# Kernel tuning notes

Measured on AMD Instinct MI355X. Metric: run time of the kernel, lower is better.

## Reference

```python
import jax, jax.numpy as jnp
import numpy as np

B, S, D, H = 2, 2048, 2048, 16
HD = D // H  # 128


def apply_rotary(xq, xk, cos, sin):
    # xq, xk: [B, S, H, HD]; cos, sin: [S, HD//2]
    def rot(x):
        xr = x.astype(jnp.float32).reshape(*x.shape[:-1], -1, 2)  # [B,S,H,HD/2,2]
        xe, xo = xr[..., 0], xr[..., 1]
        c = cos[None, :, None, :]
        s = sin[None, :, None, :]
        out_e = xe * c - xo * s
        out_o = xe * s + xo * c
        out = jnp.stack([out_e, out_o], axis=-1).reshape(x.shape)
        return out.astype(x.dtype)
    return rot(xq), rot(xk)


def setup_inputs() -> dict:
    key = jax.random.key(0)
    ks = jax.random.split(key, 8)
    x = jax.random.normal(ks[0], (B, S, D), dtype=jnp.float32)
    scale = 1.0 / np.sqrt(D)
    wq = jax.random.normal(ks[1], (D, D), dtype=jnp.float32) * scale
    wk = jax.random.normal(ks[2], (D, D), dtype=jnp.float32) * scale
    wv = jax.random.normal(ks[3], (D, D), dtype=jnp.float32) * scale
    wo = jax.random.normal(ks[4], (D, D), dtype=jnp.float32) * scale
    # RoPE frequencies (standard LLaMA): theta = 10000
    inv_freq = 1.0 / (10000.0 ** (np.arange(0, HD, 2, dtype=np.float32) / HD))
    t = np.arange(S, dtype=np.float32)
    ang = np.outer(t, inv_freq)  # [S, HD/2]
    freqs_cos = jnp.asarray(np.cos(ang))
    freqs_sin = jnp.asarray(np.sin(ang))
    # causal additive mask [1,1,S,S]
    neg = jnp.full((S, S), -1e9, dtype=jnp.float32)
    mask = jnp.triu(neg, k=1)[None, None, :, :]
    return {"x": x, "start_pos": 0, "freqs_cos": freqs_cos, "freqs_sin": freqs_sin,
            "mask": mask, "wq": wq, "wk": wk, "wv": wv, "wo": wo}


def reference(x, start_pos, freqs_cos, freqs_sin, mask, wq, wk, wv, wo):
    bsz, seqlen, dim = x.shape
    xq = (x @ wq.T).reshape(bsz, seqlen, H, HD)
    xk = (x @ wk.T).reshape(bsz, seqlen, H, HD)
    xv = (x @ wv.T).reshape(bsz, seqlen, H, HD)
    xq, xk = apply_rotary(xq, xk, freqs_cos, freqs_sin)
    # [B,H,S,HD]
    q = xq.transpose(0, 2, 1, 3)
    k = xk.transpose(0, 2, 1, 3)
    v = xv.transpose(0, 2, 1, 3)
    scores = jnp.einsum('bhqd,bhkd->bhqk', q, k) / jnp.sqrt(jnp.float32(HD))
    scores = scores + mask
    probs = jax.nn.softmax(scores.astype(jnp.float32), axis=-1).astype(q.dtype)
    out = jnp.einsum('bhqk,bhkd->bhqd', probs, v)
    out = out.transpose(0, 2, 1, 3).reshape(bsz, seqlen, dim)
    return out @ wo.T
```

## Files before the change

kernel.cpp:

```cpp
#include <hip/hip_runtime.h>
#include <cstdint>

typedef unsigned short u16;
typedef __attribute__((ext_vector_type(8))) short bf16x8;
typedef __attribute__((ext_vector_type(4))) float f32x4;

#define S_LEN 2048
#define DM    2048
#define NH    16
#define HDIM  128

__device__ __forceinline__ u16 f2bf(float f) {
  union { float f; unsigned u; } v; v.f = f;
  unsigned r = v.u + 0x7fffu + ((v.u >> 16) & 1u);
  return (u16)(r >> 16);
}
__device__ __forceinline__ float bf2f(u16 h) {
  union { unsigned u; float f; } v; v.u = ((unsigned)h) << 16;
  return v.f;
}

typedef __attribute__((address_space(3))) void lds_void_t;
typedef const __attribute__((address_space(1))) void gbl_void_t;
__device__ __forceinline__ void gload_lds16(const void* g, void* l) {
  __builtin_amdgcn_global_load_lds((gbl_void_t*)g, (lds_void_t*)l, 16, 0, 0);
}

#define VMCNTN(nn) asm volatile("s_waitcnt vmcnt(%0)" :: "n"(nn) : "memory")

__global__ void cvt5_k(const float* s0, u16* d0, int n0,
                       const float* s1, u16* d1, int n1,
                       const float* s2, u16* d2, int n2,
                       const float* s3, u16* d3, int n3,
                       const float* s4, u16* d4, int n4) {
  const int stride = gridDim.x * blockDim.x;
  const int tid = blockIdx.x * blockDim.x + threadIdx.x;
#define CVT(S, D, N)                                        \
  for (int i = tid; i < ((N) >> 2); i += stride) {          \
    float4 v = ((const float4*)(S))[i];                     \
    ushort4 o;                                              \
    o.x = f2bf(v.x); o.y = f2bf(v.y);                       \
    o.z = f2bf(v.z); o.w = f2bf(v.w);                       \
    ((ushort4*)(D))[i] = o;                                 \
  }
  CVT(s0, d0, n0) CVT(s1, d1, n1) CVT(s2, d2, n2)
  CVT(s3, d3, n3) CVT(s4, d4, n4)
#undef CVT
}

template <int BM, int BN, int M, int N, int K, typename CT, int MODE>
__global__ __launch_bounds__(512, 2) void gemm8(const u16* __restrict__ A,
                                                const u16* __restrict__ Bm,
                                                CT* __restrict__ C,
                                                const float* __restrict__ fc,
                                                const float* __restrict__ fs,
                                                u16* __restrict__ qtp,
                                                u16* __restrict__ ktp) {
  constexpr int PWM = BM / 2, PWN = BN / 4;
  constexpr int MR = PWM / 16, NR = PWN / 16, NB = NR / 2;
  constexpr int LA = BM / 128, LB = BN / 128;
  constexpr int VM = LA + LB;
  constexpr int nbn = N / BN, nbm = M / BM;
  constexpr int nwg = nbm * nbn;
  constexpr int GM = 8;
  __shared__ u16 sA[4 * BM * 32];
  __shared__ u16 sB[4 * BN * 32];

  const int t = threadIdx.x;
  const int lane = t & 63, wid = t >> 6;
  const int r0 = lane & 15, kq = lane >> 4;
  const int wr = wid >> 2, wc = wid & 3;

  const int bid = blockIdx.x;
  const int wgl = (bid & 7) * (nwg >> 3) + (bid >> 3);
  const int gid = wgl / (GM * nbn);
  const int rem = wgl % (GM * nbn);
  const long tile_m = (long)(gid * GM + (rem & (GM - 1))) * BM;
  const long tile_n = (long)(rem >> 3) * BN;

  constexpr int NT = K >> 6;
  constexpr int NITER = NT >> 1;

  const int swzcol = ((t & 3) ^ ((t >> 3) & 3)) * 8;
  const u16* gA = A + (tile_m + (t >> 2)) * (long)K + swzcol;
  const u16* gB = Bm + (tile_n + (t >> 2)) * (long)K + swzcol;

  auto stageA = [&](int kt, int kh) {
    u16* base = &sA[((kt & 1) * 2 + kh) * (BM * 32)] + wid * 512;
#pragma unroll
    for (int r = 0; r < LA; ++r)
      gload_lds16(gA + (long)(r * 128) * K + kt * 64 + kh * 32, base + r * 4096);
  };
  auto stageB = [&](int kt, int kh) {
    u16* base = &sB[((kt & 1) * 2 + kh) * (BN * 32)] + wid * 512;
#pragma unroll
    for (int r = 0; r < LB; ++r)
      gload_lds16(gB + (long)(r * 128) * K + kt * 64 + kh * 32, base + r * 4096);
  };

  const int rdslot = (kq ^ ((r0 >> 1) & 3)) * 8;
  const int aoff = (wr * PWM + r0) * 32 + rdslot;
  const int boff = (wc * PWN + r0) * 32 + rdslot;

  f32x4 acc[MR][NR];
#pragma unroll
  for (int m = 0; m < MR; ++m)
#pragma unroll
    for (int n = 0; n < NR; ++n) acc[m][n] = (f32x4){0.f, 0.f, 0.f, 0.f};

  stageA(0, 0); stageB(0, 0); stageA(0, 1); stageB(0, 1);
  stageA(1, 0); stageB(1, 0);
  VMCNTN(VM);
  __builtin_amdgcn_s_barrier();

#define PH(KT, KH, G, STAGE_STMT, VM_STMT)                                  \
  {                                                                         \
    const u16* ra = &sA[(((KT) & 1) * 2 + (KH)) * (BM * 32)] + aoff;        \
    const u16* rb = &sB[(((KT) & 1) * 2 + (KH)) * (BN * 32)] + boff;        \
    if ((G) == 0) {                                                         \
      _Pragma("unroll") for (int m = 0; m < MR; ++m)                        \
          a[m] = *(const bf16x8*)(ra + m * 512);                            \
    }                                                                       \
    _Pragma("unroll") for (int n = 0; n < NB; ++n)                          \
        b[n] = *(const bf16x8*)(rb + ((G) * NB + n) * 512);                 \
    STAGE_STMT;                                                             \
    VM_STMT;                                                                \
    __builtin_amdgcn_s_barrier();                                           \
    __builtin_amdgcn_s_setprio(1);                                          \
    _Pragma("unroll") for (int m = 0; m < MR; ++m)                          \
        _Pragma("unroll") for (int n = 0; n < NB; ++n)                      \
            acc[m][(G) * NB + n] = __builtin_amdgcn_mfma_f32_16x16x32_bf16( \
                a[m], b[n], acc[m][(G) * NB + n], 0, 0, 0);                 \
    __builtin_amdgcn_s_setprio(0);                                          \
    __builtin_amdgcn_s_barrier();                                           \
  }

  for (int it = 0; it < NITER; ++it) {
    const int kt0 = 2 * it, kt1 = 2 * it + 1;
    const bool last = (it == NITER - 1);
    bf16x8 a[MR], b[NB];
    PH(kt0, 0, 0, stageA(kt1, 1), ((void)0));
    PH(kt0, 0, 1, stageB(kt1, 1), ((void)0));
    PH(kt0, 1, 0, { if (kt0 + 2 < NT) stageA(kt0 + 2, 0); }, ((void)0));
    PH(kt0, 1, 1, { if (kt0 + 2 < NT) stageB(kt0 + 2, 0); },
       { if (last) { VMCNTN(0); } else { VMCNTN(VM); } });
    PH(kt1, 0, 0, { if (kt0 + 2 < NT) stageA(kt0 + 2, 1); }, ((void)0));
    PH(kt1, 0, 1, { if (kt0 + 2 < NT) stageB(kt0 + 2, 1); }, ((void)0));
    PH(kt1, 1, 0, { if (kt0 + 3 < NT) stageA(kt0 + 3, 0); }, ((void)0));
    PH(kt1, 1, 1, { if (kt0 + 3 < NT) stageB(kt0 + 3, 0); }, VMCNTN(VM));
  }
#undef PH

  if constexpr (MODE == 1) {
    const int z = (int)(tile_n >> 11);
    if (z == 2) {
#pragma unroll
      for (int m = 0; m < MR; ++m)
#pragma unroll
        for (int n = 0; n < NR; ++n)
#pragma unroll
          for (int r = 0; r < 4; ++r) {
            long grow = tile_m + wr * PWM + m * 16 + kq * 4 + r;
            long gcol = tile_n + wc * PWN + n * 16 + r0;
            C[grow * N + gcol] = (CT)f2bf(acc[m][n][r]);
          }
    } else {
      const float qsc = 0.12751743202f;
#pragma unroll
      for (int m = 0; m < MR; ++m)
#pragma unroll
        for (int n = 0; n < NR; ++n)
#pragma unroll
          for (int r = 0; r < 4; ++r) {
            long grow = tile_m + wr * PWM + m * 16 + kq * 4 + r;
            long gcol = tile_n + wc * PWN + n * 16 + r0;
            int srow = (int)(grow & 2047), bidx = (int)(grow >> 11);
            int h = ((int)gcol >> 7) & 15, hd = (int)gcol & 127;
            float v = acc[m][n][r];
            float partner = __shfl_xor(v, 1);
            int hd2 = hd >> 1;
            float c = fc[srow * 64 + hd2], sn = fs[srow * 64 + hd2];
            float res = (r0 & 1) ? (partner * sn + v * c)
                                 : (v * c - partner * sn);
            if (z == 0) res *= qsc;
            u16* dst = z ? ktp : qtp;
            dst[((long)(bidx * 16 + h) * S_LEN + srow) * HDIM + hd] = f2bf(res);
          }
    }
  } else {
#pragma unroll
    for (int m = 0; m < MR; ++m)
#pragma unroll
      for (int n = 0; n < NR; ++n)
#pragma unroll
        for (int r = 0; r < 4; ++r) {
          long grow = tile_m + wr * PWM + m * 16 + kq * 4 + r;
          long gcol = tile_n + wc * PWN + n * 16 + r0;
          float v = acc[m][n][r];
          if constexpr (sizeof(CT) == 2) C[grow * N + gcol] = (CT)f2bf(v);
          else                           C[grow * N + gcol] = v;
        }
  }
}

__global__ void vtrans_k(const u16* __restrict__ qkv, u16* __restrict__ vt) {
  __shared__ u16 tile[64][65];
  int bh = blockIdx.z;
  int b = bh >> 4, h = bh & 15;
  int s0 = blockIdx.x * 64, d0 = blockIdx.y * 64;
  int tx = threadIdx.x, ty = threadIdx.y;
#pragma unroll
  for (int i = 0; i < 64; i += 4) {
    int s = s0 + ty + i;
    tile[ty + i][tx] = qkv[((long)(b * S_LEN + s)) * 6144 + 4096 + h * HDIM + d0 + tx];
  }
  __syncthreads();
#pragma unroll
  for (int i = 0; i < 64; i += 4) {
    int d = d0 + ty + i;
    vt[((long)bh * HDIM + d) * S_LEN + s0 + tx] = tile[tx][ty + i];
  }
}

__global__ __launch_bounds__(128) void flash_k(const u16* __restrict__ qt,
                                               const u16* __restrict__ kt,
                                               const u16* __restrict__ vt,
                                               u16* __restrict__ attn) {
  constexpr int PS = 40;
  __shared__ u16 pbuf[2][2][32 * PS];
  const int t = threadIdx.x, lane = t & 63, wid = t >> 6;
  const int r0 = lane & 15, kq = lane >> 4;
  const int bh = blockIdx.x, b = bh >> 4, h = bh & 15;
  const int tile = (gridDim.y - 1) - blockIdx.y;
  const int q0w = tile * 64 + wid * 32;
  const int crow = kq * 4;

  const u16* qb = qt + ((long)bh * S_LEN + q0w) * HDIM;
  const u16* kb = kt + (long)bh * S_LEN * HDIM;
  const u16* vb = vt + (long)bh * HDIM * S_LEN;
  u16* pb0 = &pbuf[0][wid][0];
  u16* pb1 = &pbuf[1][wid][0];

  bf16x8 aq[2][4];
#pragma unroll
  for (int qc = 0; qc < 2; ++qc)
#pragma unroll
    for (int kk = 0; kk < 4; ++kk)
      aq[qc][kk] = *(const bf16x8*)(qb + (qc * 16 + r0) * HDIM + kk * 32 + kq * 8);

  f32x4 o[2][8];
  float mrow[2] = {-1e30f, -1e30f}, lrow[2] = {0.f, 0.f};
#pragma unroll
  for (int qc = 0; qc < 2; ++qc)
#pragma unroll
    for (int dt = 0; dt < 8; ++dt) o[qc][dt] = (f32x4){0.f, 0.f, 0.f, 0.f};

  bf16x8 bkA[2][4], bkB[2][4], bvA[8], bvB[8];
  f32x4 saccA[2][2], saccB[2][2];

  auto loadK = [&](bf16x8 (&dst)[2][4], int kv) {
#pragma unroll
    for (int kc = 0; kc < 2; ++kc)
#pragma unroll
      for (int kk = 0; kk < 4; ++kk)
        dst[kc][kk] = *(const bf16x8*)(kb + (long)(kv + kc * 16 + r0) * HDIM + kk * 32 + kq * 8);
  };
  auto loadV = [&](bf16x8 (&dst)[8], int kv) {
#pragma unroll
    for (int dt = 0; dt < 8; ++dt)
      dst[dt] = *(const bf16x8*)(vb + (long)(dt * 16 + r0) * S_LEN + kv + kq * 8);
  };
  auto qk = [&](bf16x8 (&kf)[2][4], f32x4 (&sacc)[2][2]) {
    __builtin_amdgcn_s_setprio(1);
#pragma unroll
    for (int kc = 0; kc < 2; ++kc) {
      f32x4 a0 = (f32x4){0.f, 0.f, 0.f, 0.f};
      f32x4 a1 = (f32x4){0.f, 0.f, 0.f, 0.f};
#pragma unroll
      for (int kk = 0; kk < 4; ++kk) {
        a0 = __builtin_amdgcn_mfma_f32_16x16x32_bf16(kf[kc][kk], aq[0][kk], a0, 0, 0, 0);
        a1 = __builtin_amdgcn_mfma_f32_16x16x32_bf16(kf[kc][kk], aq[1][kk], a1, 0, 0, 0);
      }
      sacc[kc][0] = a0; sacc[kc][1] = a1;
    }
    __builtin_amdgcn_s_setprio(0);
  };
  auto softmax_store = [&](f32x4 (&sacc)[2][2], int kv0, u16* pb) {
    const bool diag = (kv0 == q0w);
#pragma unroll
    for (int qc = 0; qc < 2; ++qc) {
      float s[2][4];
#pragma unroll
      for (int kc = 0; kc < 2; ++kc)
#pragma unroll
        for (int r = 0; r < 4; ++r) {
          float v = sacc[kc][qc][r];
          if (diag && (kc * 16 + crow + r > qc * 16 + r0)) v = -1e30f;
          s[kc][r] = v;
        }
      float pm = fmaxf(fmaxf(fmaxf(s[0][0], s[0][1]), fmaxf(s[0][2], s[0][3])),
                       fmaxf(fmaxf(s[1][0], s[1][1]), fmaxf(s[1][2], s[1][3])));
      pm = fmaxf(pm, __shfl_xor(pm, 16));
      pm = fmaxf(pm, __shfl_xor(pm, 32));
      if (!__all(pm - mrow[qc] <= 11.5416f)) {
        float mnew = fmaxf(mrow[qc], pm);
        float co = exp2f(mrow[qc] - mnew);
        mrow[qc] = mnew;
        lrow[qc] *= co;
        float cod[4];
#pragma unroll
        for (int r = 0; r < 4; ++r)
          cod[r] = __shfl(co, (lane & 48) | (crow + r));
#pragma unroll
        for (int dt = 0; dt < 8; ++dt)
#pragma unroll
          for (int r = 0; r < 4; ++r)
            o[qc][dt][r] *= cod[r];
      }
      float p[2][4];
      float rs = 0.f;
#pragma unroll
      for (int kc = 0; kc < 2; ++kc)
#pragma unroll
        for (int r = 0; r < 4; ++r) {
          p[kc][r] = exp2f(s[kc][r] - mrow[qc]);
          rs += p[kc][r];
        }
      rs += __shfl_xor(rs, 16);
      rs += __shfl_xor(rs, 32);
      lrow[qc] += rs;
#pragma unroll
      for (int kc = 0; kc < 2; ++kc) {
        unsigned w0, w1;
        asm("v_cvt_pk_bf16_f32 %0, %1, %2" : "=v"(w0) : "v"(p[kc][0]), "v"(p[kc][1]));
        asm("v_cvt_pk_bf16_f32 %0, %1, %2" : "=v"(w1) : "v"(p[kc][2]), "v"(p[kc][3]));
        uint2 w; w.x = w0; w.y = w1;
        *(uint2*)(pb + (qc * 16 + r0) * PS + kc * 16 + crow) = w;
      }
    }
  };
  auto pv = [&](const u16* pb, bf16x8 (&bv)[8]) {
    bf16x8 pa0 = *(const bf16x8*)(pb + r0 * PS + kq * 8);
    bf16x8 pa1 = *(const bf16x8*)(pb + (16 + r0) * PS + kq * 8);
    __builtin_amdgcn_s_setprio(1);
#pragma unroll
    for (int dt = 0; dt < 8; ++dt) {
      o[0][dt] = __builtin_amdgcn_mfma_f32_16x16x32_bf16(pa0, bv[dt], o[0][dt], 0, 0, 0);
      o[1][dt] = __builtin_amdgcn_mfma_f32_16x16x32_bf16(pa1, bv[dt], o[1][dt], 0, 0, 0);
    }
    __builtin_amdgcn_s_setprio(0);
  };

  loadK(bkA, 0);
  if (32 <= q0w) loadK(bkB, 32);
  qk(bkA, saccA);
  int kv0 = 0;
  for (;;) {
    {
      const bool more = (kv0 + 32 <= q0w);
      loadV(bvA, kv0);
      softmax_store(saccA, kv0, pb0);
      if (more) qk(bkB, saccB);
      if (kv0 + 64 <= q0w) loadK(bkA, kv0 + 64);
      pv(pb0, bvA);
      kv0 += 32;
      if (!more) break;
    }
    {
      const bool more = (kv0 + 32 <= q0w);
      loadV(bvB, kv0);
      softmax_store(saccB, kv0, pb1);
      if (more) qk(bkA, saccA);
      if (kv0 + 64 <= q0w) loadK(bkB, kv0 + 64);
      pv(pb1, bvB);
      kv0 += 32;
      if (!more) break;
    }
  }

#pragma unroll
  for (int qc = 0; qc < 2; ++qc) {
    float linv[4];
#pragma unroll
    for (int r = 0; r < 4; ++r)
      linv[r] = 1.0f / __shfl(lrow[qc], (lane & 48) | (crow + r));
#pragma unroll
    for (int dt = 0; dt < 8; ++dt)
#pragma unroll
      for (int r = 0; r < 4; ++r) {
        int srow = q0w + qc * 16 + crow + r;
        attn[((long)(b * S_LEN + srow)) * DM + h * HDIM + dt * 16 + r0] =
            f2bf(o[qc][dt][r] * linv[r]);
      }
  }
}

extern "C" void kernel_launch(void* const* d_in, const int* in_sizes, int n_in,
                              void* d_out, int out_size, void* d_ws, size_t ws_size,
                              hipStream_t stream) {
  (void)in_sizes; (void)n_in; (void)out_size; (void)ws_size;
  const float* x  = (const float*)d_in[0];
  const float* fc = (const float*)d_in[2];
  const float* fs = (const float*)d_in[3];
  const float* wq = (const float*)d_in[5];
  const float* wk = (const float*)d_in[6];
  const float* wv = (const float*)d_in[7];
  const float* wo = (const float*)d_in[8];
  float* out = (float*)d_out;

  u16* xb   = (u16*)d_ws;
  u16* wqkv = xb + 8388608;
  u16* wob  = wqkv + 12582912;
  u16* qkv  = wob + 4194304;
  u16* qt   = qkv + 25165824;
  u16* kt   = qt + 8388608;
  u16* vt   = kt + 8388608;
  u16* attn = qkv;

  cvt5_k<<<2048, 256, 0, stream>>>(x, xb, 8388608,
                                   wq, wqkv, 4194304,
                                   wk, wqkv + 4194304, 4194304,
                                   wv, wqkv + 8388608, 4194304,
                                   wo, wob, 4194304);

  gemm8<128, 256, 4096, 6144, 2048, u16, 1><<<768, 512, 0, stream>>>(
      xb, wqkv, qkv, fc, fs, qt, kt);

  vtrans_k<<<dim3(32, 2, 32), dim3(64, 4), 0, stream>>>(qkv, vt);

  flash_k<<<dim3(32, 32), 128, 0, stream>>>(qt, kt, vt, attn);

  gemm8<128, 256, 4096, 2048, 2048, float, 0><<<256, 512, 0, stream>>>(
      attn, wob, out, nullptr, nullptr, nullptr, nullptr);
}
```

Baseline: 316.9 us.

## Merge GEMM main-loop half-phases into four full-width phases with deeper prefetch

The GEMM main loop is restructured from eight half-width phases per iteration (each loading half the B fragments and staging one of A or B) into four full-width phases. Each phase now loads all A and B fragments, stages both A and B for a future k-slice, and waits with a larger outstanding-load count. This halves the number of barriers per iteration and keeps more global loads in flight. In exchange it doubles the live B fragment registers under a 512-thread, 2-block launch bound, which risks spills. It also drops the end-of-K bounds checks and the final full drain, so the last iterations issue prefetches past K.

```diff
diff --git a/kernel.cpp b/kernel.cpp
--- a/kernel.cpp
+++ b/kernel.cpp
@@ -57,9 +57,9 @@
                                                 u16* __restrict__ qtp,
                                                 u16* __restrict__ ktp) {
   constexpr int PWM = BM / 2, PWN = BN / 4;
-  constexpr int MR = PWM / 16, NR = PWN / 16, NB = NR / 2;
+  constexpr int MR = PWM / 16, NR = PWN / 16;
   constexpr int LA = BM / 128, LB = BN / 128;
-  constexpr int VM = LA + LB;
+  constexpr int VM6 = 2 * (LA + LB);
   constexpr int nbn = N / BN, nbm = M / BM;
   constexpr int nwg = nbm * nbn;
   constexpr int GM = 8;
@@ -110,46 +110,39 @@
 
   stageA(0, 0); stageB(0, 0); stageA(0, 1); stageB(0, 1);
   stageA(1, 0); stageB(1, 0);
-  VMCNTN(VM);
+  VMCNTN(VM6);
   __builtin_amdgcn_s_barrier();
 
-#define PH(KT, KH, G, STAGE_STMT, VM_STMT)                                  \
+#define PH4(KT, KH, SKT, SKH)                                               \
   {                                                                         \
     const u16* ra = &sA[(((KT) & 1) * 2 + (KH)) * (BM * 32)] + aoff;        \
     const u16* rb = &sB[(((KT) & 1) * 2 + (KH)) * (BN * 32)] + boff;        \
-    if ((G) == 0) {                                                         \
-      _Pragma("unroll") for (int m = 0; m < MR; ++m)                        \
-          a[m] = *(const bf16x8*)(ra + m * 512);                            \
-    }                                                                       \
-    _Pragma("unroll") for (int n = 0; n < NB; ++n)                          \
-        b[n] = *(const bf16x8*)(rb + ((G) * NB + n) * 512);                 \
-    STAGE_STMT;                                                             \
-    VM_STMT;                                                                \
+    _Pragma("unroll") for (int m = 0; m < MR; ++m)                          \
+        a[m] = *(const bf16x8*)(ra + m * 512);                              \
+    _Pragma("unroll") for (int n = 0; n < NR; ++n)                          \
+        b[n] = *(const bf16x8*)(rb + n * 512);                              \
+    stageA(SKT, SKH);                                                       \
+    stageB(SKT, SKH);                                                       \
+    VMCNTN(VM6);                                                            \
     __builtin_amdgcn_s_barrier();                                           \
     __builtin_amdgcn_s_setprio(1);                                          \
     _Pragma("unroll") for (int m = 0; m < MR; ++m)                          \
-        _Pragma("unroll") for (int n = 0; n < NB; ++n)                      \
-            acc[m][(G) * NB + n] = __builtin_amdgcn_mfma_f32_16x16x32_bf16( \
-                a[m], b[n], acc[m][(G) * NB + n], 0, 0, 0);                 \
+        _Pragma("unroll") for (int n = 0; n < NR; ++n)                      \
+            acc[m][n] = __builtin_amdgcn_mfma_f32_16x16x32_bf16(            \
+                a[m], b[n], acc[m][n], 0, 0, 0);                            \
     __builtin_amdgcn_s_setprio(0);                                          \
     __builtin_amdgcn_s_barrier();                                           \
   }
 
   for (int it = 0; it < NITER; ++it) {
     const int kt0 = 2 * it, kt1 = 2 * it + 1;
-    const bool last = (it == NITER - 1);
-    bf16x8 a[MR], b[NB];
-    PH(kt0, 0, 0, stageA(kt1, 1), ((void)0));
-    PH(kt0, 0, 1, stageB(kt1, 1), ((void)0));
-    PH(kt0, 1, 0, { if (kt0 + 2 < NT) stageA(kt0 + 2, 0); }, ((void)0));
-    PH(kt0, 1, 1, { if (kt0 + 2 < NT) stageB(kt0 + 2, 0); },
-       { if (last) { VMCNTN(0); } else { VMCNTN(VM); } });
-    PH(kt1, 0, 0, { if (kt0 + 2 < NT) stageA(kt0 + 2, 1); }, ((void)0));
-    PH(kt1, 0, 1, { if (kt0 + 2 < NT) stageB(kt0 + 2, 1); }, ((void)0));
-    PH(kt1, 1, 0, { if (kt0 + 3 < NT) stageA(kt0 + 3, 0); }, ((void)0));
-    PH(kt1, 1, 1, { if (kt0 + 3 < NT) stageB(kt0 + 3, 0); }, VMCNTN(VM));
-  }
-#undef PH
+    bf16x8 a[MR], b[NR];
+    PH4(kt0, 0, kt1, 1);
+    PH4(kt0, 1, kt0 + 2, 0);
+    PH4(kt1, 0, kt0 + 2, 1);
+    PH4(kt1, 1, kt0 + 3, 0);
+  }
+#undef PH4
 
   if constexpr (MODE == 1) {
     const int z = (int)(tile_n >> 11);
```

Result: no change. 316.6 us (-0.1%).

## Fuse V transpose into QKV GEMM epilogue and prefetch V one step ahead

Applied to the files above, without the earlier changes.

The QKV projection GEMM now writes V tiles transposed directly into the vt buffer by staging them through shared memory in the epilogue. This removes the separate vtrans kernel launch and its extra read and write of V. The flash attention loop also loads the next V block one iteration early, using the double buffers, so the load latency overlaps with softmax and QK work. In exchange, the epilogue reuses the GEMM's LDS and adds a barrier, and V is no longer written to the qkv buffer.

```diff
diff --git a/kernel.cpp b/kernel.cpp
--- a/kernel.cpp
+++ b/kernel.cpp
@@ -55,16 +55,19 @@
                                                 const float* __restrict__ fc,
                                                 const float* __restrict__ fs,
                                                 u16* __restrict__ qtp,
-                                                u16* __restrict__ ktp) {
+                                                u16* __restrict__ ktp,
+                                                u16* __restrict__ vtp) {
   constexpr int PWM = BM / 2, PWN = BN / 4;
   constexpr int MR = PWM / 16, NR = PWN / 16, NB = NR / 2;
   constexpr int LA = BM / 128, LB = BN / 128;
   constexpr int VM = LA + LB;
+  constexpr int SASZ = 4 * BM * 32;
   constexpr int nbn = N / BN, nbm = M / BM;
   constexpr int nwg = nbm * nbn;
   constexpr int GM = 8;
-  __shared__ u16 sA[4 * BM * 32];
-  __shared__ u16 sB[4 * BN * 32];
+  __shared__ u16 smem[SASZ + 4 * BN * 32];
+  u16* sA = smem;
+  u16* sB = smem + SASZ;
 
   const int t = threadIdx.x;
   const int lane = t & 63, wid = t >> 6;
@@ -154,16 +157,28 @@
   if constexpr (MODE == 1) {
     const int z = (int)(tile_n >> 11);
     if (z == 2) {
+      u16* tb = smem;
 #pragma unroll
       for (int m = 0; m < MR; ++m)
 #pragma unroll
-        for (int n = 0; n < NR; ++n)
-#pragma unroll
-          for (int r = 0; r < 4; ++r) {
-            long grow = tile_m + wr * PWM + m * 16 + kq * 4 + r;
-            long gcol = tile_n + wc * PWN + n * 16 + r0;
-            C[grow * N + gcol] = (CT)f2bf(acc[m][n][r]);
-          }
+        for (int n = 0; n < NR; ++n) {
+          int row0 = wr * PWM + m * 16 + kq * 4;
+          int col  = wc * PWN + n * 16 + r0;
+          ushort4 pk;
+          pk.x = f2bf(acc[m][n][0]); pk.y = f2bf(acc[m][n][1]);
+          pk.z = f2bf(acc[m][n][2]); pk.w = f2bf(acc[m][n][3]);
+          *(ushort4*)(tb + col * 132 + row0) = pk;
+        }
+      __builtin_amdgcn_s_barrier();
+      const int bidx = (int)(tile_m >> 11), s0 = (int)(tile_m & 2047);
+#pragma unroll 4
+      for (int it2 = 0; it2 < 32; ++it2) {
+        int col = it2 * 8 + wid;
+        long gc = tile_n + col;
+        int h2 = ((int)gc >> 7) & 15, hd2 = (int)gc & 127;
+        unsigned vv = *(const unsigned*)(tb + col * 132 + 2 * lane);
+        *(unsigned*)(vtp + ((long)(bidx * 16 + h2) * HDIM + hd2) * S_LEN + s0 + 2 * lane) = vv;
+      }
     } else {
       const float qsc = 0.12751743202f;
 #pragma unroll
@@ -203,25 +218,6 @@
   }
 }
 
-__global__ void vtrans_k(const u16* __restrict__ qkv, u16* __restrict__ vt) {
-  __shared__ u16 tile[64][65];
-  int bh = blockIdx.z;
-  int b = bh >> 4, h = bh & 15;
-  int s0 = blockIdx.x * 64, d0 = blockIdx.y * 64;
-  int tx = threadIdx.x, ty = threadIdx.y;
-#pragma unroll
-  for (int i = 0; i < 64; i += 4) {
-    int s = s0 + ty + i;
-    tile[ty + i][tx] = qkv[((long)(b * S_LEN + s)) * 6144 + 4096 + h * HDIM + d0 + tx];
-  }
-  __syncthreads();
-#pragma unroll
-  for (int i = 0; i < 64; i += 4) {
-    int d = d0 + ty + i;
-    vt[((long)bh * HDIM + d) * S_LEN + s0 + tx] = tile[tx][ty + i];
-  }
-}
-
 __global__ __launch_bounds__(128) void flash_k(const u16* __restrict__ qt,
                                                const u16* __restrict__ kt,
                                                const u16* __restrict__ vt,
@@ -353,12 +349,13 @@
 
   loadK(bkA, 0);
   if (32 <= q0w) loadK(bkB, 32);
+  loadV(bvA, 0);
   qk(bkA, saccA);
   int kv0 = 0;
   for (;;) {
     {
       const bool more = (kv0 + 32 <= q0w);
-      loadV(bvA, kv0);
+      if (more) loadV(bvB, kv0 + 32);
       softmax_store(saccA, kv0, pb0);
       if (more) qk(bkB, saccB);
       if (kv0 + 64 <= q0w) loadK(bkA, kv0 + 64);
@@ -368,7 +365,7 @@
     }
     {
       const bool more = (kv0 + 32 <= q0w);
-      loadV(bvB, kv0);
+      if (more) loadV(bvA, kv0 + 32);
       softmax_store(saccB, kv0, pb1);
       if (more) qk(bkA, saccA);
       if (kv0 + 64 <= q0w) loadK(bkB, kv0 + 64);
@@ -424,12 +421,10 @@
                                    wo, wob, 4194304);
 
   gemm8<128, 256, 4096, 6144, 2048, u16, 1><<<768, 512, 0, stream>>>(
-      xb, wqkv, qkv, fc, fs, qt, kt);
-
-  vtrans_k<<<dim3(32, 2, 32), dim3(64, 4), 0, stream>>>(qkv, vt);
+      xb, wqkv, qkv, fc, fs, qt, kt, vt);
 
   flash_k<<<dim3(32, 32), 128, 0, stream>>>(qt, kt, vt, attn);
 
   gemm8<128, 256, 4096, 2048, 2048, float, 0><<<256, 512, 0, stream>>>(
-      attn, wob, out, nullptr, nullptr, nullptr, nullptr);
-}
+      attn, wob, out, nullptr, nullptr, nullptr, nullptr, nullptr);
+}
```

New measurement: 288.6 us (median of 3 runs). 1.1x faster.
